# Kernel tuning notes

Measured on AMD Instinct MI355X. Metric: run time of the kernel, lower is better.

The kernel has to match this reference:

```python
import jax, jax.numpy as jnp
import numpy as np
import math

N, E = 100000, 1600000
IN_FEATS, H, Z_DIM, D, B_COEF = 128, 128, 32, 2, 0.2


def calc_thetas(d):
    # Bernstein-basis thetas, ascending coefficients (matches calculate_theta2)
    thetas = []
    for i in range(d + 1):
        p1 = np.zeros(i + 1); p1[i] = 0.5 ** i               # (x/2)^i
        p2 = np.array([math.comb(d - i, j) * (-0.5) ** j for j in range(d - i + 1)])  # (1-x/2)^(d-i)
        coeffs = np.convolve(p1, p2)                          # length d+1, ascending
        beta = math.gamma(i + 1) * math.gamma(d + 1 - i) / math.gamma(d + 2)
        thetas.append((coeffs / beta).tolist())
    return thetas

THETAS = calc_thetas(D)


def linear(x, w, b):
    return x @ w.T + b


def polyconv(theta, feat, src, dst, d_invsqrt, n):
    h = theta[0] * feat
    for k in range(1, len(theta)):
        tmp = feat * d_invsqrt                                # [N, F]
        agg = jax.ops.segment_sum(tmp[src], dst, num_segments=n)
        feat = feat - agg * d_invsqrt                         # (I - D^-1/2 A D^-1/2) feat
        h = h + theta[k] * feat
    return h


def enc_dec(x, w1, b1, w2, b2, src, dst, d_invsqrt, n):
    x = jax.nn.relu(linear(x, w1, b1))
    hs = jnp.concatenate([polyconv(t, x, src, dst, d_invsqrt, n) for t in THETAS], axis=-1)
    return linear(hs, w2, b2)


def setup_inputs() -> dict:
    key = jax.random.key(0)
    ks = jax.random.split(key, 16)
    nb = len(THETAS)
    return {
        "features": jax.random.normal(ks[0], (N, IN_FEATS), jnp.float32),
        "src": jax.random.randint(ks[1], (E,), 0, N, jnp.int32),
        "dst": jax.random.randint(ks[2], (E,), 0, N, jnp.int32),
        "enc_w1": jax.random.normal(ks[3], (H, IN_FEATS), jnp.float32) * 0.05,
        "enc_b1": jnp.zeros((H,), jnp.float32),
        "enc_w2": jax.random.normal(ks[4], (H, H * nb), jnp.float32) * 0.05,
        "enc_b2": jnp.zeros((H,), jnp.float32),
        "dec_w1": jax.random.normal(ks[5], (IN_FEATS, H), jnp.float32) * 0.05,
        "dec_b1": jnp.zeros((IN_FEATS,), jnp.float32),
        "dec_w2": jax.random.normal(ks[6], (IN_FEATS, IN_FEATS * nb), jnp.float32) * 0.05,
        "dec_b2": jnp.zeros((IN_FEATS,), jnp.float32),
        "rep_w": jax.random.normal(ks[7], (Z_DIM, H), jnp.float32) * 0.05,
        "rep_b": jnp.zeros((Z_DIM,), jnp.float32),
        "rec_w": jax.random.normal(ks[8], (H, Z_DIM), jnp.float32) * 0.05,
        "rec_b": jnp.zeros((H,), jnp.float32),
        "disc_w": jax.random.uniform(ks[9], (H, H), jnp.float32, -1.0 / math.sqrt(H), 1.0 / math.sqrt(H)),
    }


def reference(features, src, dst, enc_w1, enc_b1, enc_w2, enc_b2,
              dec_w1, dec_b1, dec_w2, dec_b2, rep_w, rep_b, rec_w, rec_b, disc_w):
    n = features.shape[0]
    degs = jax.ops.segment_sum(jnp.ones((src.shape[0],), jnp.float32), dst, num_segments=n)
    d_invsqrt = jnp.maximum(degs, 1.0) ** -0.5
    d_invsqrt = d_invsqrt[:, None]

    positive = enc_dec(features, enc_w1, enc_b1, enc_w2, enc_b2, src, dst, d_invsqrt, n)
    perm = jax.random.permutation(jax.random.key(7), n)
    negative = enc_dec(features[perm], enc_w1, enc_b1, enc_w2, enc_b2, src, dst, d_invsqrt, n)

    summary = jax.nn.sigmoid(positive.mean(axis=0))           # [H]
    pos_dis = positive @ (disc_w @ summary)                   # [N]
    neg_dis = negative @ (disc_w @ summary)
    # BCEWithLogits: target=1 -> softplus(-x); target=0 -> softplus(x)
    dgi_loss = jnp.mean(jax.nn.softplus(-pos_dis)) + jnp.mean(jax.nn.softplus(neg_dis))

    mu = linear(positive, rep_w, rep_b)
    log_var = mu
    eps = jax.random.normal(jax.random.key(11), mu.shape, mu.dtype)
    z = mu + eps * jnp.exp(log_var / 2)

    x_rec = enc_dec(linear(z, rec_w, rec_b), dec_w1, dec_b1, dec_w2, dec_b2, src, dst, d_invsqrt, n)
    reconst_loss = jnp.sum((x_rec - features) ** 2)
    kl_div = -0.5 * jnp.sum(1 + log_var - mu ** 2 - jnp.exp(log_var))
    vgae_loss = reconst_loss + kl_div

    ratio = jax.lax.stop_gradient(dgi_loss / vgae_loss)
    return B_COEF * dgi_loss / ratio + (1 - B_COEF) * vgae_loss
```

## Files before the change

### kernel.cpp

```cpp
#include <hip/hip_runtime.h>
#include <math.h>

#define NN   100000
#define EE   1600000
#define F    128
#define ZD   32
#define SCAN_B 256
#define PREP_BLOCKS 161
#define FC1_BLOCKS  1563
#define ENC_BLOCKS  1563
#define NBUCK 391
#define PART_CHUNK 8192
#define PART_BLOCKS 196


typedef float f32x4 __attribute__((ext_vector_type(4)));
typedef int   i32x4 __attribute__((ext_vector_type(4)));
typedef __bf16 bf16x8 __attribute__((ext_vector_type(8)));

__device__ __forceinline__ f32x4 mfma16(i32x4 a, i32x4 b, f32x4 c) {
    return __builtin_amdgcn_mfma_f32_16x16x32_bf16(
        __builtin_bit_cast(bf16x8, a), __builtin_bit_cast(bf16x8, b), c, 0, 0, 0);
}

__device__ __forceinline__ unsigned f2bf(float f) {
    unsigned u = __float_as_uint(f);
    return (u + 0x7fffu + ((u >> 16) & 1u)) >> 16;
}
__device__ __forceinline__ float bf2f(unsigned h) { return __uint_as_float(h << 16); }

__device__ __forceinline__ unsigned pcg_hash(unsigned v) {
    v = v * 747796405u + 2891336453u;
    unsigned w = ((v >> ((v >> 28u) + 4u)) ^ v) * 277803737u;
    return (w >> 22u) ^ w;
}

__device__ __forceinline__ float block_reduce_sum(float v) {
    #pragma unroll
    for (int o = 32; o > 0; o >>= 1) v += __shfl_down(v, o, 64);
    __shared__ float s[8];
    int lane = threadIdx.x & 63, w = threadIdx.x >> 6;
    if (lane == 0) s[w] = v;
    __syncthreads();
    float t = 0.f;
    if (threadIdx.x == 0) {
        int nw = (blockDim.x + 63) >> 6;
        for (int i = 0; i < nw; ++i) t += s[i];
    }
    return t;
}

__global__ __launch_bounds__(256) void prep_deg_kernel(
        const float* __restrict__ repw, const float* __restrict__ w2e,
        const float* __restrict__ b2e,  const float* __restrict__ repb,
        const float* __restrict__ w2d,
        const float* __restrict__ w1d,  const float* __restrict__ recw,
        const float* __restrict__ recb, const float* __restrict__ b1d,
        const float* __restrict__ w1e,
        unsigned short* __restrict__ Wcat,
        float* __restrict__ bmu,
        unsigned short* __restrict__ wd2_a,
        unsigned short* __restrict__ wd2_b,
        unsigned short* __restrict__ wd2_c,
        unsigned short* __restrict__ wrd,
        float* __restrict__ brd,
        unsigned short* __restrict__ w1bf,
        const int* __restrict__ dst, int* __restrict__ degs, int e) {
    int bid = blockIdx.x, tid = threadIdx.x;
    if (bid >= PREP_BLOCKS) {
        int i = (bid - PREP_BLOCKS) * 256 + tid;
        if (i < e) atomicAdd(&degs[dst[i]], 1);
        return;
    }
    if (bid < 16) {
        int idx = bid * 256 + tid;
        int i = idx >> 7, k = idx & 127;
        float m0 = 0.f, m1 = 0.f, m2 = 0.f;
        for (int h = 0; h < 128; ++h) {
            float r = repw[i * 128 + h];
            const float* wr = w2e + (size_t)h * 384 + k;
            m0 += r * wr[0];
            m1 += r * wr[128];
            m2 += r * wr[256];
        }
        Wcat[(size_t)i * 128 + k]        = (unsigned short)f2bf(3.f * m0);
        Wcat[(size_t)(32 + i) * 128 + k] = (unsigned short)f2bf(3.f * (m1 - m0));
        Wcat[(size_t)(64 + i) * 128 + k] = (unsigned short)f2bf(0.75f * m0 - 1.5f * m1 + 0.75f * m2);
    } else if (bid == 16) {
        if (tid < 32) {
            float s = repb[tid];
            for (int h = 0; h < 128; ++h) s += repw[tid * 128 + h] * b2e[h];
            bmu[tid] = s;
        }
    } else if (bid < 81) {
        int idx = (bid - 17) * 256 + tid;
        int j = idx >> 7, k = idx & 127;
        const float* wr = w2d + (size_t)j * 384 + k;
        float w0 = wr[0], w1 = wr[128], w2v = wr[256];
        wd2_a[idx] = (unsigned short)f2bf(3.f * w0);
        wd2_b[idx] = (unsigned short)f2bf(3.f * (w1 - w0));
        wd2_c[idx] = (unsigned short)f2bf(0.75f * w0 - 1.5f * w1 + 0.75f * w2v);
    } else if (bid < 97) {
        int idx = (bid - 81) * 256 + tid;
        int j = idx >> 5, i = idx & 31;
        float s = 0.f;
        for (int h = 0; h < 128; ++h) s += w1d[j * 128 + h] * recw[h * 32 + i];
        wrd[idx] = (unsigned short)f2bf(s);
        if (idx < 128) {
            float b = b1d[idx];
            for (int h = 0; h < 128; ++h) b += w1d[idx * 128 + h] * recb[h];
            brd[idx] = b;
        }
    } else {
        int idx = (bid - 97) * 256 + tid;
        w1bf[idx] = (unsigned short)f2bf(w1e[idx]);
    }
}

__global__ __launch_bounds__(SCAN_B) void scan_block_kernel(const int* __restrict__ degs,
                                                            int* __restrict__ rowstart,
                                                            int* __restrict__ blocksums,
                                                            float* __restrict__ dinv,
                                                            float* __restrict__ rsq, int n) {
    __shared__ int sh[SCAN_B];
    int i = blockIdx.x * SCAN_B + threadIdx.x;
    int v = (i < n) ? degs[i] : 0;
    int pd = (v + 15) & ~15;
    sh[threadIdx.x] = pd;
    __syncthreads();
    for (int o = 1; o < SCAN_B; o <<= 1) {
        int t = (threadIdx.x >= o) ? sh[threadIdx.x - o] : 0;
        __syncthreads();
        sh[threadIdx.x] += t;
        __syncthreads();
    }
    if (i < n) {
        rowstart[i] = sh[threadIdx.x] - pd;
        float d = fmaxf((float)v, 1.f);
        float s = sqrtf(d);
        rsq[i] = s;
        dinv[i] = 1.f / s;
    }
    if (threadIdx.x == SCAN_B - 1) blocksums[blockIdx.x] = sh[threadIdx.x];
}

__global__ __launch_bounds__(512) void scan_sums_kernel(int* __restrict__ blocksums, int nb) {
    __shared__ int sh[512];
    int v = (threadIdx.x < nb) ? blocksums[threadIdx.x] : 0;
    sh[threadIdx.x] = v;
    __syncthreads();
    for (int o = 1; o < 512; o <<= 1) {
        int t = (threadIdx.x >= o) ? sh[threadIdx.x - o] : 0;
        __syncthreads();
        sh[threadIdx.x] += t;
        __syncthreads();
    }
    if (threadIdx.x < nb) blocksums[threadIdx.x] = sh[threadIdx.x] - v;
}

__global__ __launch_bounds__(SCAN_B) void scan_add_kernel(int* __restrict__ rowstart,
                                                          int* __restrict__ cursor,
                                                          const int* __restrict__ blocksums,
                                                          const int* __restrict__ degs,
                                                          int* __restrict__ csr_src,
                                                          int* __restrict__ bstart,
                                                          int* __restrict__ bcursor,
                                                          int n) {
    int i = blockIdx.x * SCAN_B + threadIdx.x;
    if (i < n) {
        int v = rowstart[i] + blocksums[blockIdx.x];
        rowstart[i] = v;
        cursor[i] = v;
        int d = degs[i];
        int pd = (d + 15) & ~15;
        for (int j = d; j < pd; ++j) csr_src[v + j] = n;
        if ((i & 255) == 0) { bstart[i >> 8] = v; bcursor[i >> 8] = v; }
        if (i == n - 1) rowstart[n] = v + pd;
    }
}

__global__ __launch_bounds__(256) void fc1_part_kernel(const float* __restrict__ x,
                                                       const unsigned short* __restrict__ wbf,
                                                       const float* __restrict__ b,
                                                       unsigned short* __restrict__ out,
                                                       const int* __restrict__ src,
                                                       const int* __restrict__ dst,
                                                       int* __restrict__ bcursor,
                                                       int* __restrict__ ebuf,
                                                       int n, int e) {
    if (blockIdx.x >= FC1_BLOCKS) {
        __shared__ int hist[NBUCK], lofs[NBUCK], gbase[NBUCK];
        int pid = blockIdx.x - FC1_BLOCKS;
        int e0 = pid * PART_CHUNK;
        int e1 = min(e0 + PART_CHUNK, e);
        int tid = threadIdx.x;
        for (int bb = tid; bb < NBUCK; bb += 256) hist[bb] = 0;
        __syncthreads();
        for (int i = e0 + tid; i < e1; i += 256) atomicAdd(&hist[dst[i] >> 8], 1);
        __syncthreads();
        for (int bb = tid; bb < NBUCK; bb += 256) {
            int cct = hist[bb];
            gbase[bb] = cct ? atomicAdd(&bcursor[bb], cct) : 0;
            lofs[bb] = 0;
        }
        __syncthreads();
        for (int i = e0 + tid; i < e1; i += 256) {
            int d = dst[i];
            int bb = d >> 8;
            int pos = gbase[bb] + atomicAdd(&lofs[bb], 1);
            ebuf[pos] = (src[i] << 8) | (d & 255);
        }
        return;
    }
    int wv = threadIdx.x >> 6, lane = threadIdx.x & 63;
    int l16 = lane & 15, lhi = lane >> 4;
    int rowbase = blockIdx.x * 64 + wv * 16;
    int arow = rowbase + l16;
    f32x4 acc[8];
    #pragma unroll
    for (int jt = 0; jt < 8; ++jt) {
        float bj = b[jt * 16 + l16];
        acc[jt] = (f32x4){bj, bj, bj, bj};
    }
    #pragma unroll
    for (int kk = 0; kk < 4; ++kk) {
        int kbase = kk * 32 + lhi * 8;
        i32x4 afrag = {0, 0, 0, 0};
        if (arow < n) {
            const float* ap = x + (size_t)arow * F + kbase;
            f32x4 f0 = *reinterpret_cast<const f32x4*>(ap);
            f32x4 f1 = *reinterpret_cast<const f32x4*>(ap + 4);
            afrag.x = (int)(f2bf(f0.x) | (f2bf(f0.y) << 16));
            afrag.y = (int)(f2bf(f0.z) | (f2bf(f0.w) << 16));
            afrag.z = (int)(f2bf(f1.x) | (f2bf(f1.y) << 16));
            afrag.w = (int)(f2bf(f1.z) | (f2bf(f1.w) << 16));
        }
        #pragma unroll
        for (int jt = 0; jt < 8; ++jt) {
            i32x4 bfrag = *reinterpret_cast<const i32x4*>(wbf + (size_t)(jt * 16 + l16) * F + kbase);
            acc[jt] = mfma16(afrag, bfrag, acc[jt]);
        }
    }
    #pragma unroll
    for (int jt = 0; jt < 8; ++jt)
        #pragma unroll
        for (int r = 0; r < 4; ++r) {
            int row = rowbase + lhi * 4 + r;
            if (row < n)
                out[(size_t)row * F + jt * 16 + l16] =
                    (unsigned short)f2bf(fmaxf(acc[jt][r], 0.f));
        }
}

__global__ __launch_bounds__(256) void encproj_csr_kernel(const unsigned short* __restrict__ A,
                                                          const unsigned short* __restrict__ Wcat,
                                                          const float* __restrict__ dinv,
                                                          unsigned short* __restrict__ G0,
                                                          unsigned short* __restrict__ G1s,
                                                          unsigned short* __restrict__ G2s,
                                                          const int* __restrict__ ebuf,
                                                          const int* __restrict__ bstart,
                                                          const int* __restrict__ bend,
                                                          int* __restrict__ cursor,
                                                          int* __restrict__ csr_src,
                                                          int n) {
    if (blockIdx.x >= ENC_BLOCKS) {
        int bb = blockIdx.x - ENC_BLOCKS;
        int s0 = bstart[bb], s1 = bend[bb];
        for (int i = s0 + (int)threadIdx.x; i < s1; i += 256) {
            int p = ebuf[i];
            int d = (bb << 8) | (p & 255);
            int pos = atomicAdd(&cursor[d], 1);
            csr_src[pos] = p >> 8;
        }
        return;
    }
    int wv = threadIdx.x >> 6, lane = threadIdx.x & 63;
    int l16 = lane & 15, lhi = lane >> 4;
    int rowbase = blockIdx.x * 64 + wv * 16;
    int arow = rowbase + l16;
    float dv[4];
    #pragma unroll
    for (int r = 0; r < 4; ++r) {
        int row = rowbase + lhi * 4 + r;
        dv[r] = (row < n) ? dinv[row] : 1.f;
    }
    f32x4 acc[6];
    #pragma unroll
    for (int jt = 0; jt < 6; ++jt) acc[jt] = (f32x4){0.f, 0.f, 0.f, 0.f};
    #pragma unroll
    for (int kk = 0; kk < 4; ++kk) {
        int kbase = kk * 32 + lhi * 8;
        i32x4 afrag = {0, 0, 0, 0};
        if (arow < n)
            afrag = *reinterpret_cast<const i32x4*>(A + (size_t)arow * F + kbase);
        #pragma unroll
        for (int jt = 0; jt < 6; ++jt) {
            i32x4 bfrag = *reinterpret_cast<const i32x4*>(Wcat + (size_t)(jt * 16 + l16) * F + kbase);
            acc[jt] = mfma16(afrag, bfrag, acc[jt]);
        }
    }
    #pragma unroll
    for (int jt = 0; jt < 6; ++jt)
        #pragma unroll
        for (int r = 0; r < 4; ++r) {
            int row = rowbase + lhi * 4 + r;
            int j = jt * 16 + l16;
            if (row < n) {
                if (j < 32) {
                    G0[(size_t)row * 32 + j] = (unsigned short)f2bf(acc[jt][r]);
                } else if (j < 64) {
                    G1s[(size_t)row * 32 + (j - 32)] = (unsigned short)f2bf(acc[jt][r] * dv[r]);
                } else {
                    G2s[(size_t)row * 32 + (j - 64)] = (unsigned short)f2bf(acc[jt][r] * dv[r]);
                }
            }
        }
}

__global__ __launch_bounds__(256) void gather32_W_kernel(const unsigned short* __restrict__ G2s,
                                                         const unsigned short* __restrict__ G1s,
                                                         const int* __restrict__ csr_src,
                                                         const int* __restrict__ rowstart,
                                                         const float* __restrict__ dinv,
                                                         unsigned short* __restrict__ W, int n) {
    int g = threadIdx.x >> 4;
    int lane = threadIdx.x & 15;
    int r0 = blockIdx.x * 32 + g * 2;
    if (r0 >= n) return;
    int c = lane * 2;
    int start = rowstart[r0];
    int mid   = rowstart[r0 + 1];
    int end   = rowstart[r0 + 2];
    int pd0 = mid - start;
    int total = end - start;
    float ax0 = 0.f, ay0 = 0.f, ax1 = 0.f, ay1 = 0.f;
    for (int base = 0; base < total; base += 16) {
        int s = csr_src[start + base + lane];
        unsigned v[16];
        #pragma unroll
        for (int q = 0; q < 16; ++q) {
            int sq = __shfl(s, q, 16);
            v[q] = *reinterpret_cast<const unsigned*>(G2s + (size_t)sq * 32 + c);
        }
        #pragma unroll
        for (int q = 0; q < 16; ++q) {
            float vx = bf2f(v[q] & 0xffffu), vy = bf2f(v[q] >> 16);
            if (base + q < pd0) { ax0 += vx; ay0 += vy; }
            else                { ax1 += vx; ay1 += vy; }
        }
    }
    {
        float di = dinv[r0], di2 = di * di;
        unsigned g2v = *reinterpret_cast<const unsigned*>(G2s + (size_t)r0 * 32 + c);
        unsigned g1v = *reinterpret_cast<const unsigned*>(G1s + (size_t)r0 * 32 + c);
        float wx = bf2f(g1v & 0xffffu) + bf2f(g2v & 0xffffu) - di2 * ax0;
        float wy = bf2f(g1v >> 16)     + bf2f(g2v >> 16)     - di2 * ay0;
        *reinterpret_cast<unsigned*>(W + (size_t)r0 * 32 + c) = f2bf(wx) | (f2bf(wy) << 16);
    }
    if (r0 + 1 < n) {
        int r1 = r0 + 1;
        float di = dinv[r1], di2 = di * di;
        unsigned g2v = *reinterpret_cast<const unsigned*>(G2s + (size_t)r1 * 32 + c);
        unsigned g1v = *reinterpret_cast<const unsigned*>(G1s + (size_t)r1 * 32 + c);
        float wx = bf2f(g1v & 0xffffu) + bf2f(g2v & 0xffffu) - di2 * ax1;
        float wy = bf2f(g1v >> 16)     + bf2f(g2v >> 16)     - di2 * ay1;
        *reinterpret_cast<unsigned*>(W + (size_t)r1 * 32 + c) = f2bf(wx) | (f2bf(wy) << 16);
    }
}

__global__ __launch_bounds__(256) void gather32_mukl_kernel(const unsigned short* __restrict__ W,
                                                            const unsigned short* __restrict__ G0,
                                                            const int* __restrict__ csr_src,
                                                            const int* __restrict__ rowstart,
                                                            const float* __restrict__ dinv,
                                                            const float* __restrict__ rsq,
                                                            const float* __restrict__ bmu,
                                                            unsigned short* __restrict__ Z,
                                                            double* __restrict__ accd, int n) {
    int g = threadIdx.x >> 4;
    int lane = threadIdx.x & 15;
    int r0 = blockIdx.x * 32 + g * 2;
    int c = lane * 2;
    float kl = 0.f;
    if (r0 < n) {
        int start = rowstart[r0];
        int mid   = rowstart[r0 + 1];
        int end   = rowstart[r0 + 2];
        int pd0 = mid - start;
        int total = end - start;
        float axs0 = 0.f, ays0 = 0.f, axs1 = 0.f, ays1 = 0.f;
        for (int base = 0; base < total; base += 16) {
            int s = csr_src[start + base + lane];
            unsigned v[16];
            #pragma unroll
            for (int q = 0; q < 16; ++q) {
                int sq = __shfl(s, q, 16);
                v[q] = *reinterpret_cast<const unsigned*>(W + (size_t)sq * 32 + c);
            }
            #pragma unroll
            for (int q = 0; q < 16; ++q) {
                float vx = bf2f(v[q] & 0xffffu), vy = bf2f(v[q] >> 16);
                if (base + q < pd0) { axs0 += vx; ays0 += vy; }
                else                { axs1 += vx; ays1 += vy; }
            }
        }
        float axs[2] = {axs0, axs1}, ays[2] = {ays0, ays1};
        #pragma unroll
        for (int rr = 0; rr < 2; ++rr) {
            int r = r0 + rr;
            if (r < n) {
                float di = dinv[r];
                float rs = rsq[r];
                unsigned wv = *reinterpret_cast<const unsigned*>(W + (size_t)r * 32 + c);
                unsigned g0v = *reinterpret_cast<const unsigned*>(G0 + (size_t)r * 32 + c);
                float mu0 = bf2f(g0v & 0xffffu) + rs * bf2f(wv & 0xffffu) - di * axs[rr] + bmu[c];
                float mu1 = bf2f(g0v >> 16)     + rs * bf2f(wv >> 16)     - di * ays[rr] + bmu[c + 1];
                kl += (1.f + mu0 - mu0 * mu0 - expf(mu0)) + (1.f + mu1 - mu1 * mu1 - expf(mu1));
                unsigned idx0 = (unsigned)(r * ZD + c);
                unsigned h1 = pcg_hash(2u * idx0 + 1u);
                unsigned h2 = pcg_hash(2u * idx0 + 2u);
                float u1 = ((float)h1 + 0.5f) * 2.3283064365386963e-10f;
                float u2 = ((float)h2 + 0.5f) * 2.3283064365386963e-10f;
                float eps0 = sqrtf(-2.f * logf(u1)) * cosf(6.283185307179586f * u2);
                unsigned idx1 = idx0 + 1u;
                unsigned h3 = pcg_hash(2u * idx1 + 1u);
                unsigned h4 = pcg_hash(2u * idx1 + 2u);
                float u3 = ((float)h3 + 0.5f) * 2.3283064365386963e-10f;
                float u4 = ((float)h4 + 0.5f) * 2.3283064365386963e-10f;
                float eps1 = sqrtf(-2.f * logf(u3)) * cosf(6.283185307179586f * u4);
                float z0 = mu0 + eps0 * expf(0.5f * mu0);
                float z1 = mu1 + eps1 * expf(0.5f * mu1);
                *reinterpret_cast<unsigned*>(Z + (size_t)r * ZD + c) = f2bf(z0) | (f2bf(z1) << 16);
            }
        }
    }
    float bs = block_reduce_sum(kl);
    if (threadIdx.x == 0) atomicAdd(&accd[1], (double)bs);
}

__global__ __launch_bounds__(256) void gather128_kernel(const unsigned short* __restrict__ x,
                                                        const int* __restrict__ csr_src,
                                                        const int* __restrict__ rowstart,
                                                        const float* __restrict__ dinv,
                                                        unsigned short* __restrict__ out, int n) {
    int r = blockIdx.x * 4 + (threadIdx.x >> 6);
    if (r >= n) return;
    int lane = threadIdx.x & 63;
    int c = lane * 2;
    int start = rowstart[r];
    int total = rowstart[r + 1] - start;
    float ax = 0.f, ay = 0.f;
    for (int base = 0; base < total; base += 16) {
        int s = csr_src[start + base + (lane & 15)];
        unsigned v[16];
        #pragma unroll
        for (int q = 0; q < 16; ++q) {
            int sq = __shfl(s, q, 16);
            v[q] = *reinterpret_cast<const unsigned*>(x + (size_t)sq * F + c);
        }
        #pragma unroll
        for (int q = 0; q < 16; ++q) {
            ax += bf2f(v[q] & 0xffffu);
            ay += bf2f(v[q] >> 16);
        }
    }
    float di = dinv[r];
    float di2 = di * di;
    unsigned xv = *reinterpret_cast<const unsigned*>(x + (size_t)r * F + c);
    float ox = bf2f(xv & 0xffffu) - di2 * ax;
    float oy = bf2f(xv >> 16) - di2 * ay;
    *reinterpret_cast<unsigned*>(out + (size_t)r * F + c) = f2bf(ox) | (f2bf(oy) << 16);
}

__global__ __launch_bounds__(256) void recdec1_mfma_kernel(const unsigned short* __restrict__ Z,
                                                           const unsigned short* __restrict__ Wrd,
                                                           const float* __restrict__ brd,
                                                           const float* __restrict__ dinv,
                                                           unsigned short* __restrict__ out, int n) {
    int wv = threadIdx.x >> 6, lane = threadIdx.x & 63;
    int l16 = lane & 15, lhi = lane >> 4;
    int rowbase = blockIdx.x * 64 + wv * 16;
    int arow = rowbase + l16;
    int kbase = lhi * 8;
    float dv[4];
    #pragma unroll
    for (int r = 0; r < 4; ++r) {
        int row = rowbase + lhi * 4 + r;
        dv[r] = (row < n) ? dinv[row] : 1.f;
    }
    i32x4 afrag = {0, 0, 0, 0};
    if (arow < n)
        afrag = *reinterpret_cast<const i32x4*>(Z + (size_t)arow * ZD + kbase);
    #pragma unroll
    for (int jt = 0; jt < 8; ++jt) {
        float bj = brd[jt * 16 + l16];
        f32x4 acc = (f32x4){bj, bj, bj, bj};
        i32x4 bfrag = *reinterpret_cast<const i32x4*>(Wrd + (size_t)(jt * 16 + l16) * ZD + kbase);
        acc = mfma16(afrag, bfrag, acc);
        #pragma unroll
        for (int r = 0; r < 4; ++r) {
            int row = rowbase + lhi * 4 + r;
            if (row < n)
                out[(size_t)row * F + jt * 16 + l16] =
                    (unsigned short)f2bf(fmaxf(acc[r], 0.f) * dv[r]);
        }
    }
}

__global__ __launch_bounds__(256) void dec2loss_mfma_kernel(const unsigned short* __restrict__ A,
                                                            const unsigned short* __restrict__ B,
                                                            const unsigned short* __restrict__ C,
                                                            const unsigned short* __restrict__ Wa,
                                                            const unsigned short* __restrict__ Wb,
                                                            const unsigned short* __restrict__ Wc,
                                                            const float* __restrict__ b2,
                                                            const float* __restrict__ rsq,
                                                            const float* __restrict__ feats,
                                                            double* __restrict__ accd, int n) {
    __shared__ __align__(16) unsigned short wsh[128 * 128];
    int tid = threadIdx.x;
    int wv = tid >> 6, lane = tid & 63;
    int l16 = lane & 15, lhi = lane >> 4;
    int rowbase = blockIdx.x * 64 + wv * 16;
    int arow = rowbase + l16;
    float fpre[8][4];
    float rsv[4];
    #pragma unroll
    for (int r = 0; r < 4; ++r) {
        int row = rowbase + lhi * 4 + r;
        rsv[r] = (row < n) ? rsq[row] : 1.f;
    }
    #pragma unroll
    for (int jt = 0; jt < 8; ++jt)
        #pragma unroll
        for (int r = 0; r < 4; ++r) {
            int row = rowbase + lhi * 4 + r;
            fpre[jt][r] = (row < n) ? feats[(size_t)row * F + jt * 16 + l16] : 0.f;
        }
    f32x4 acc[8];
    #pragma unroll
    for (int jt = 0; jt < 8; ++jt) acc[jt] = (f32x4){0.f, 0.f, 0.f, 0.f};
    const unsigned short* mats[3] = {A, B, C};
    const unsigned short* wsrc[3] = {Wa, Wb, Wc};
    #pragma unroll
    for (int s = 0; s < 3; ++s) {
        __syncthreads();
        #pragma unroll
        for (int it = 0; it < 8; ++it) {
            int idx = it * 256 + tid;
            int j = idx >> 4;
            int colb = (idx & 15) << 4;
            i32x4 v = *reinterpret_cast<const i32x4*>(wsrc[s] + (size_t)j * 128 + ((idx & 15) << 3));
            *reinterpret_cast<i32x4*>((char*)wsh + j * 256 + (colb ^ ((j & 7) << 4))) = v;
        }
        __syncthreads();
        #pragma unroll
        for (int kk = 0; kk < 4; ++kk) {
            i32x4 afrag = {0, 0, 0, 0};
            if (arow < n)
                afrag = *reinterpret_cast<const i32x4*>(mats[s] + (size_t)arow * F + kk * 32 + lhi * 8);
            #pragma unroll
            for (int jt = 0; jt < 8; ++jt) {
                int j = jt * 16 + l16;
                int colb = (kk * 64 + lhi * 16) ^ ((j & 7) << 4);
                i32x4 bfrag = *reinterpret_cast<const i32x4*>((const char*)wsh + j * 256 + colb);
                acc[jt] = mfma16(afrag, bfrag, acc[jt]);
            }
        }
    }
    float local = 0.f;
    #pragma unroll
    for (int jt = 0; jt < 8; ++jt) {
        float bj = b2[jt * 16 + l16];
        #pragma unroll
        for (int r = 0; r < 4; ++r) {
            int row = rowbase + lhi * 4 + r;
            if (row < n) {
                float d = acc[jt][r] * rsv[r] + bj - fpre[jt][r];
                local += d * d;
            }
        }
    }
    float bs = block_reduce_sum(local);
    if (threadIdx.x == 0) atomicAdd(&accd[0], (double)bs);
}

__global__ void finalize_kernel(const double* __restrict__ acc, float* __restrict__ out) {
    out[0] = (float)(acc[0] - 0.5 * acc[1]);
}

extern "C" void kernel_launch(void* const* d_in, const int* in_sizes, int n_in,
                              void* d_out, int out_size, void* d_ws, size_t ws_size,
                              hipStream_t stream) {
    const float* feats  = (const float*)d_in[0];
    const int*   src    = (const int*)d_in[1];
    const int*   dst    = (const int*)d_in[2];
    const float* enc_w1 = (const float*)d_in[3];
    const float* enc_b1 = (const float*)d_in[4];
    const float* enc_w2 = (const float*)d_in[5];
    const float* enc_b2 = (const float*)d_in[6];
    const float* dec_w1 = (const float*)d_in[7];
    const float* dec_b1 = (const float*)d_in[8];
    const float* dec_w2 = (const float*)d_in[9];
    const float* dec_b2 = (const float*)d_in[10];
    const float* rep_w  = (const float*)d_in[11];
    const float* rep_b  = (const float*)d_in[12];
    const float* rec_w  = (const float*)d_in[13];
    const float* rec_b  = (const float*)d_in[14];

    const int n = NN, e = EE;
    char* ws = (char*)d_ws;
    size_t off = 0;
    auto alloc = [&](size_t bytes) -> void* {
        void* p = ws + off;
        off += (bytes + 255) & ~(size_t)255;
        return p;
    };
    const size_t NFB = (size_t)(n + 1) * F * sizeof(unsigned short);
    const size_t N32 = (size_t)(n + 1) * 32 * sizeof(unsigned short);
    const int nScanBlocks = (n + SCAN_B - 1) / SCAN_B;
    const int csrCap = e + 15 * NN + 64;
    int*    degs    = (int*)alloc((size_t)n * sizeof(int));
    float*  dinv    = (float*)alloc((size_t)n * sizeof(float));
    float*  rsq     = (float*)alloc((size_t)n * sizeof(float));
    int*    rowst   = (int*)alloc((size_t)(n + 1) * sizeof(int));
    int*    cursor  = (int*)alloc((size_t)n * sizeof(int));
    int*    bsums   = (int*)alloc((size_t)nScanBlocks * sizeof(int));
    int*    bstart  = (int*)alloc((NBUCK + 1) * sizeof(int));
    int*    bcursor = (int*)alloc(NBUCK * sizeof(int));
    int*    ebuf    = (int*)alloc((size_t)csrCap * sizeof(int));
    int*    csr_src = (int*)alloc((size_t)csrCap * sizeof(int));
    unsigned short* Abf = (unsigned short*)alloc(NFB);
    unsigned short* Bbf = (unsigned short*)alloc(NFB);
    unsigned short* Cbf = (unsigned short*)alloc((size_t)n * F * sizeof(unsigned short));
    unsigned short* G0  = (unsigned short*)alloc(N32);
    unsigned short* G1  = (unsigned short*)alloc(N32);
    unsigned short* G2  = (unsigned short*)alloc(N32);
    unsigned short* Wg  = (unsigned short*)alloc(N32);
    unsigned short* Zbf = (unsigned short*)alloc((size_t)n * ZD * sizeof(unsigned short));
    unsigned short* Wcat  = (unsigned short*)alloc(96 * 128 * sizeof(unsigned short));
    unsigned short* w1bf  = (unsigned short*)alloc(128 * 128 * sizeof(unsigned short));
    unsigned short* wd2_a = (unsigned short*)alloc(128 * 128 * sizeof(unsigned short));
    unsigned short* wd2_b = (unsigned short*)alloc(128 * 128 * sizeof(unsigned short));
    unsigned short* wd2_c = (unsigned short*)alloc(128 * 128 * sizeof(unsigned short));
    unsigned short* wrd   = (unsigned short*)alloc(128 * 32 * sizeof(unsigned short));
    float* bmu = (float*)alloc(32 * sizeof(float));
    float* brd = (float*)alloc(128 * sizeof(float));
    double* acc = (double*)alloc(2 * sizeof(double));

    const int gemm64   = (n + 63) / 64;
    const int csrBlks  = (e + 255) / 256;
    const int gathBlks = (n + 3) / 4;
    const int g32Blks  = (n + 31) / 32;

    hipMemsetAsync(degs, 0, (size_t)n * sizeof(int), stream);
    hipMemsetAsync(acc, 0, 2 * sizeof(double), stream);
    hipMemsetAsync(Abf + (size_t)n * F, 0, F * sizeof(unsigned short), stream);
    hipMemsetAsync(Bbf + (size_t)n * F, 0, F * sizeof(unsigned short), stream);
    hipMemsetAsync(G2 + (size_t)n * 32, 0, 32 * sizeof(unsigned short), stream);
    hipMemsetAsync(Wg + (size_t)n * 32, 0, 32 * sizeof(unsigned short), stream);

    prep_deg_kernel<<<PREP_BLOCKS + csrBlks, 256, 0, stream>>>(
        rep_w, enc_w2, enc_b2, rep_b, dec_w2, dec_w1, rec_w, rec_b, dec_b1, enc_w1,
        Wcat, bmu, wd2_a, wd2_b, wd2_c, wrd, brd, w1bf, dst, degs, e);

    scan_block_kernel<<<nScanBlocks, SCAN_B, 0, stream>>>(degs, rowst, bsums, dinv, rsq, n);
    scan_sums_kernel<<<1, 512, 0, stream>>>(bsums, nScanBlocks);
    scan_add_kernel<<<nScanBlocks, SCAN_B, 0, stream>>>(rowst, cursor, bsums, degs,
                                                        csr_src, bstart, bcursor, n);

    fc1_part_kernel<<<FC1_BLOCKS + PART_BLOCKS, 256, 0, stream>>>(
        feats, w1bf, enc_b1, Abf, src, dst, bcursor, ebuf, n, e);

    encproj_csr_kernel<<<ENC_BLOCKS + NBUCK, 256, 0, stream>>>(
        Abf, Wcat, dinv, G0, G1, G2, ebuf, bstart, bcursor, cursor, csr_src, n);

    gather32_W_kernel<<<g32Blks, 256, 0, stream>>>(G2, G1, csr_src, rowst, dinv, Wg, n);
    gather32_mukl_kernel<<<g32Blks, 256, 0, stream>>>(Wg, G0, csr_src, rowst, dinv,
                                                      rsq, bmu, Zbf, acc, n);

    recdec1_mfma_kernel<<<gemm64, 256, 0, stream>>>(Zbf, wrd, brd, dinv, Abf, n);
    gather128_kernel<<<gathBlks, 256, 0, stream>>>(Abf, csr_src, rowst, dinv, Bbf, n);
    gather128_kernel<<<gathBlks, 256, 0, stream>>>(Bbf, csr_src, rowst, dinv, Cbf, n);
    dec2loss_mfma_kernel<<<gemm64, 256, 0, stream>>>(Abf, Bbf, Cbf, wd2_a, wd2_b, wd2_c,
                                                     dec_b2, rsq, feats, acc, n);

    finalize_kernel<<<1, 1, 0, stream>>>(acc, (float*)d_out);
}
```

Baseline: 461.6 us.

## Fuse second decoder gather into dec2loss kernel via shared-memory tile

Removes the second gather128 launch and the Cbf intermediate buffer. dec2loss now computes the propagated features for its 64-row tile directly from the CSR neighbor lists into shared memory, then feeds them to the third MFMA stage. Also shrinks the edge partition chunk size and raises the partition block count. The trade is a global write plus read of an N×128 bf16 tensor and one launch, against extra shared memory (lower occupancy) and a gather phase inside the GEMM kernel, which may serialize latency.

```diff
diff --git a/kernel.cpp b/kernel.cpp
--- a/kernel.cpp
+++ b/kernel.cpp
@@ -10,8 +10,8 @@
 #define FC1_BLOCKS  1563
 #define ENC_BLOCKS  1563
 #define NBUCK 391
-#define PART_CHUNK 8192
-#define PART_BLOCKS 196
+#define PART_CHUNK 2048
+#define PART_BLOCKS 782
 
 
 typedef float f32x4 __attribute__((ext_vector_type(4)));
@@ -510,7 +510,9 @@
 
 __global__ __launch_bounds__(256) void dec2loss_mfma_kernel(const unsigned short* __restrict__ A,
                                                             const unsigned short* __restrict__ B,
-                                                            const unsigned short* __restrict__ C,
+                                                            const int* __restrict__ csr_src,
+                                                            const int* __restrict__ rowstart,
+                                                            const float* __restrict__ dinv,
                                                             const unsigned short* __restrict__ Wa,
                                                             const unsigned short* __restrict__ Wb,
                                                             const unsigned short* __restrict__ Wc,
@@ -519,11 +521,46 @@
                                                             const float* __restrict__ feats,
                                                             double* __restrict__ accd, int n) {
     __shared__ __align__(16) unsigned short wsh[128 * 128];
+    __shared__ __align__(16) unsigned short csh[64 * 128];
     int tid = threadIdx.x;
     int wv = tid >> 6, lane = tid & 63;
     int l16 = lane & 15, lhi = lane >> 4;
     int rowbase = blockIdx.x * 64 + wv * 16;
     int arow = rowbase + l16;
+
+    {
+        int c = lane * 2;
+        for (int rr = wv; rr < 64; rr += 4) {
+            int r = blockIdx.x * 64 + rr;
+            unsigned val = 0u;
+            if (r < n) {
+                int start = rowstart[r];
+                int total = rowstart[r + 1] - start;
+                float ax = 0.f, ay = 0.f;
+                for (int base = 0; base < total; base += 16) {
+                    int s = csr_src[start + base + (lane & 15)];
+                    unsigned v[16];
+                    #pragma unroll
+                    for (int q = 0; q < 16; ++q) {
+                        int sq = __shfl(s, q, 16);
+                        v[q] = *reinterpret_cast<const unsigned*>(B + (size_t)sq * F + c);
+                    }
+                    #pragma unroll
+                    for (int q = 0; q < 16; ++q) {
+                        ax += bf2f(v[q] & 0xffffu);
+                        ay += bf2f(v[q] >> 16);
+                    }
+                }
+                float di = dinv[r], di2 = di * di;
+                unsigned xv = *reinterpret_cast<const unsigned*>(B + (size_t)r * F + c);
+                float ox = bf2f(xv & 0xffffu) - di2 * ax;
+                float oy = bf2f(xv >> 16) - di2 * ay;
+                val = f2bf(ox) | (f2bf(oy) << 16);
+            }
+            *reinterpret_cast<unsigned*>((char*)csh + rr * 256 + ((lane * 4) ^ ((rr & 7) << 4))) = val;
+        }
+    }
+
     float fpre[8][4];
     float rsv[4];
     #pragma unroll
@@ -541,7 +578,7 @@
     f32x4 acc[8];
     #pragma unroll
     for (int jt = 0; jt < 8; ++jt) acc[jt] = (f32x4){0.f, 0.f, 0.f, 0.f};
-    const unsigned short* mats[3] = {A, B, C};
+    const unsigned short* mats[2] = {A, B};
     const unsigned short* wsrc[3] = {Wa, Wb, Wc};
     #pragma unroll
     for (int s = 0; s < 3; ++s) {
@@ -558,8 +595,14 @@
         #pragma unroll
         for (int kk = 0; kk < 4; ++kk) {
             i32x4 afrag = {0, 0, 0, 0};
-            if (arow < n)
-                afrag = *reinterpret_cast<const i32x4*>(mats[s] + (size_t)arow * F + kk * 32 + lhi * 8);
+            if (s < 2) {
+                if (arow < n)
+                    afrag = *reinterpret_cast<const i32x4*>(mats[s] + (size_t)arow * F + kk * 32 + lhi * 8);
+            } else {
+                int rl = wv * 16 + l16;
+                int colb = (kk * 64 + lhi * 16) ^ ((rl & 7) << 4);
+                afrag = *reinterpret_cast<const i32x4*>((const char*)csh + rl * 256 + colb);
+            }
             #pragma unroll
             for (int jt = 0; jt < 8; ++jt) {
                 int j = jt * 16 + l16;
@@ -633,7 +676,6 @@
     int*    csr_src = (int*)alloc((size_t)csrCap * sizeof(int));
     unsigned short* Abf = (unsigned short*)alloc(NFB);
     unsigned short* Bbf = (unsigned short*)alloc(NFB);
-    unsigned short* Cbf = (unsigned short*)alloc((size_t)n * F * sizeof(unsigned short));
     unsigned short* G0  = (unsigned short*)alloc(N32);
     unsigned short* G1  = (unsigned short*)alloc(N32);
     unsigned short* G2  = (unsigned short*)alloc(N32);
@@ -682,8 +724,8 @@
 
     recdec1_mfma_kernel<<<gemm64, 256, 0, stream>>>(Zbf, wrd, brd, dinv, Abf, n);
     gather128_kernel<<<gathBlks, 256, 0, stream>>>(Abf, csr_src, rowst, dinv, Bbf, n);
-    gather128_kernel<<<gathBlks, 256, 0, stream>>>(Bbf, csr_src, rowst, dinv, Cbf, n);
-    dec2loss_mfma_kernel<<<gemm64, 256, 0, stream>>>(Abf, Bbf, Cbf, wd2_a, wd2_b, wd2_c,
+    dec2loss_mfma_kernel<<<gemm64, 256, 0, stream>>>(Abf, Bbf, csr_src, rowst, dinv,
+                                                     wd2_a, wd2_b, wd2_c,
                                                      dec_b2, rsq, feats, acc, n);
 
     finalize_kernel<<<1, 1, 0, stream>>>(acc, (float*)d_out);
```

New measurement: 479.6 us. +3.9%, slower.
